# Kernel tuning notes

Measured on AMD Instinct MI355X. Metric: run time of the kernel, lower is better.

Reference implementation:

```python
import jax, jax.numpy as jnp
import numpy as np

DIM = 384          # input_dim
DI = 2 * DIM       # minGRU inner dim (expansion_factor=2)
MLP = 4 * DIM      # mlp_ratio=4
N, H, W = 32, 32, 32
EPS = 1e-5


def layer_norm(x, gamma, beta):
    mu = jnp.mean(x, axis=-1, keepdims=True)
    var = jnp.var(x, axis=-1, keepdims=True)
    return (x - mu) * jax.lax.rsqrt(var + EPS) * gamma + beta


def log_g(x):
    # log of g(x) = where(x>=0, x+0.5, sigmoid(x))
    return jnp.where(x >= 0, jnp.log(jax.nn.relu(x) + 0.5), -jax.nn.softplus(-x))


def min_gru(x, w_hg, w_out):
    # x: [n, L, d]; w_hg: [d, 2*di]; w_out: [di, d]
    hg = x @ w_hg
    hidden, gate = jnp.split(hg, 2, axis=-1)
    log_coeffs = -jax.nn.softplus(gate)            # log(1 - z)
    log_values = -jax.nn.softplus(-gate) + log_g(hidden)  # log z + log g(h~)
    # Heinsen associative scan in log space
    a_star = jnp.cumsum(log_coeffs, axis=1)
    log_h = a_star + jax.lax.cumlogsumexp(log_values - a_star, axis=1)
    return jnp.exp(log_h) @ w_out


def setup_inputs():
    key = jax.random.key(0)
    ks = jax.random.split(key, 10)
    r = lambda k, s, sc=0.02: jax.random.normal(k, s, jnp.float32) * sc
    return dict(
        x=jax.random.normal(ks[0], (N, H * W, DIM), jnp.float32),
        gamma1=jnp.ones((DIM,), jnp.float32), beta1=jnp.zeros((DIM,), jnp.float32),
        dwc_w=r(ks[1], (DIM, 1, 3, 3), 0.1), dwc_b=jnp.zeros((DIM,), jnp.float32),
        gru1_w=r(ks[2], (DIM, 2 * DI)), gru1_out=r(ks[3], (DI, DIM)),
        gru2_w=r(ks[4], (DIM, 2 * DI)), gru2_out=r(ks[5], (DI, DIM)),
        gamma2=jnp.ones((DIM,), jnp.float32), beta2=jnp.zeros((DIM,), jnp.float32),
        p1_w=r(ks[6], (DIM, MLP)), p1_b=jnp.zeros((MLP,), jnp.float32),
        p2_w=r(ks[7], (MLP, DIM)), p2_b=jnp.zeros((DIM,), jnp.float32),
        h=H, w=W,
    )


def reference(x, gamma1, beta1, dwc_w, dwc_b, gru1_w, gru1_out, gru2_w, gru2_out,
              gamma2, beta2, p1_w, p1_b, p2_w, p2_b, h, w):
    n = x.shape[0]
    residual = x
    xn = layer_norm(x, gamma1, beta1)
    # depthwise 3x3 conv on the 2D grid
    xg = xn.reshape(n, h, w, DIM).transpose(0, 3, 1, 2)  # NCHW
    xg = jax.lax.conv_general_dilated(
        xg, dwc_w, window_strides=(1, 1), padding=[(1, 1), (1, 1)],
        dimension_numbers=('NCHW', 'OIHW', 'NCHW'), feature_group_count=DIM)
    xg = xg + dwc_b[None, :, None, None]
    xs = xg.reshape(n, DIM, h * w).transpose(0, 2, 1)    # [n, hw, d]
    # bidirectional minGRU: reversed copy (flip both h and w == full seq reversal)
    x_rev = xs[:, ::-1, :]
    x1 = min_gru(xs, gru1_w, gru1_out)
    x2 = min_gru(x_rev, gru2_w, gru2_out)[:, ::-1, :]
    y = x1 + x2 + residual
    # MLP block
    residual = y
    yn = layer_norm(y, gamma2, beta2)
    yh = jax.nn.gelu(yn @ p1_w + p1_b, approximate=False)
    y = yh @ p2_w + p2_b + residual
    return y
```

## Files before the change

kernel.cpp:

```cpp
#include <hip/hip_runtime.h>
#include <hip/hip_bf16.h>

#define DIM 384
#define DI 768
#define S_LEN 1024
#define NB 32
#define M_ROWS (NB * S_LEN)
#define MLP_DIM 1536
#define CHUNKS 32
#define CLEN (S_LEN / CHUNKS)

typedef __bf16 bf16x8 __attribute__((ext_vector_type(8)));
typedef float f32x4 __attribute__((ext_vector_type(4)));

#define GLOBAL_AS __attribute__((address_space(1)))
#define LDS_AS __attribute__((address_space(3)))

template <typename OutT>
__global__ __launch_bounds__(256) void ln_kernel(const float* __restrict__ x,
                                                 const float* __restrict__ gamma,
                                                 const float* __restrict__ beta,
                                                 OutT* __restrict__ out) {
    int row = blockIdx.x * 4 + (threadIdx.x >> 6);
    int lane = threadIdx.x & 63;
    const float* xr = x + (size_t)row * DIM;
    float v[6];
    float s = 0.f, sq = 0.f;
#pragma unroll
    for (int i = 0; i < 6; ++i) {
        v[i] = xr[lane + i * 64];
        s += v[i];
        sq += v[i] * v[i];
    }
#pragma unroll
    for (int off = 32; off > 0; off >>= 1) {
        s += __shfl_down(s, off);
        sq += __shfl_down(sq, off);
    }
    s = __shfl(s, 0);
    sq = __shfl(sq, 0);
    float mean = s * (1.f / DIM);
    float var = sq * (1.f / DIM) - mean * mean;
    float rstd = rsqrtf(var + 1e-5f);
    OutT* orow = out + (size_t)row * DIM;
#pragma unroll
    for (int i = 0; i < 6; ++i) {
        int c = lane + i * 64;
        float y = (v[i] - mean) * rstd * gamma[c] + beta[c];
        if constexpr (sizeof(OutT) == 2)
            orow[c] = __float2bfloat16(y);
        else
            orow[c] = y;
    }
}

__global__ __launch_bounds__(256) void dwconv_kernel(const __hip_bfloat16* __restrict__ xn,
                                                     const float* __restrict__ w,
                                                     const float* __restrict__ b,
                                                     __hip_bfloat16* __restrict__ xs) {
    const int CB = DIM / 8;
    size_t tid = (size_t)blockIdx.x * 256 + threadIdx.x;
    int cb = (int)(tid % CB);
    int s = (int)((tid / CB) % S_LEN);
    int n = (int)(tid / ((size_t)CB * S_LEN));
    int c = cb * 8;
    int h0 = s >> 5, w0 = s & 31;

    float wv[72];
    {
        const float4* wp = (const float4*)(w + (size_t)c * 9);
#pragma unroll
        for (int i = 0; i < 18; ++i) ((float4*)wv)[i] = wp[i];
    }
    float acc[8];
    {
        const float4 b0 = *(const float4*)&b[c];
        const float4 b1 = *(const float4*)&b[c + 4];
        acc[0] = b0.x; acc[1] = b0.y; acc[2] = b0.z; acc[3] = b0.w;
        acc[4] = b1.x; acc[5] = b1.y; acc[6] = b1.z; acc[7] = b1.w;
    }

    const __hip_bfloat16* base = xn + (size_t)n * S_LEN * DIM + c;
#pragma unroll
    for (int kh = 0; kh < 3; ++kh) {
        int hh = h0 + kh - 1;
        if (hh < 0 || hh > 31) continue;
#pragma unroll
        for (int kw = 0; kw < 3; ++kw) {
            int ww = w0 + kw - 1;
            if (ww < 0 || ww > 31) continue;
            bf16x8 xv = *(const bf16x8*)&base[(size_t)(hh * 32 + ww) * DIM];
#pragma unroll
            for (int e = 0; e < 8; ++e)
                acc[e] += (float)xv[e] * wv[e * 9 + kh * 3 + kw];
        }
    }
    bf16x8 ov;
#pragma unroll
    for (int e = 0; e < 8; ++e) ov[e] = (__bf16)acc[e];
    *(bf16x8*)&xs[tid * 8] = ov;
}

__global__ __launch_bounds__(256) void transpose_bf16_kernel(const float* __restrict__ in,
                                                             __hip_bfloat16* __restrict__ out,
                                                             int R, int C, int ostride, int ooff) {
    int idx = blockIdx.x * 256 + threadIdx.x;
    if (idx >= R * C) return;
    int r = idx / C, c = idx % C;
    out[(size_t)c * ostride + ooff + r] = __float2bfloat16(in[idx]);
}

__device__ __forceinline__ void gru_ab(float hid, float gate, float& a, float& bv) {
    float z = 1.f / (1.f + __expf(-gate));
    float gh = (hid >= 0.f) ? (hid + 0.5f) : (1.f / (1.f + __expf(-hid)));
    a = 1.f - z;
    bv = z * gh;
}

__global__ __launch_bounds__(256) void scan_part1(const __hip_bfloat16* __restrict__ hg,
                                                  float* __restrict__ summ, int rev) {
    int tid = blockIdx.x * 256 + threadIdx.x;
    int c = tid % DI;
    int j = (tid / DI) % CHUNKS;
    int b = tid / (DI * CHUNKS);
    const __hip_bfloat16* base = hg + (size_t)b * S_LEN * (2 * DI);
    float A = 1.f, Bv = 0.f;
    for (int i = 0; i < CLEN; i += 8) {
        float hid[8], gate[8];
#pragma unroll
        for (int q = 0; q < 8; ++q) {
            int pos = j * CLEN + i + q;
            int t = rev ? (S_LEN - 1 - pos) : pos;
            hid[q] = __bfloat162float(base[(size_t)t * (2 * DI) + c]);
            gate[q] = __bfloat162float(base[(size_t)t * (2 * DI) + DI + c]);
        }
#pragma unroll
        for (int q = 0; q < 8; ++q) {
            float a, bv;
            gru_ab(hid[q], gate[q], a, bv);
            A *= a;
            Bv = a * Bv + bv;
        }
    }
    int idx = (j * NB + b) * DI + c;
    summ[idx] = A;
    summ[(size_t)CHUNKS * NB * DI + idx] = Bv;
}

__global__ __launch_bounds__(256) void scan_part2(const __hip_bfloat16* __restrict__ hg,
                                                  const float* __restrict__ summ,
                                                  __hip_bfloat16* __restrict__ ho, int rev,
                                                  int ostride) {
    int tid = blockIdx.x * 256 + threadIdx.x;
    int c = tid % DI;
    int j = (tid / DI) % CHUNKS;
    int b = tid / (DI * CHUNKS);
    const float* sB = summ + (size_t)CHUNKS * NB * DI;
    float h = 0.f;
    for (int jp = 0; jp < j; ++jp) {
        int idx = (jp * NB + b) * DI + c;
        h = summ[idx] * h + sB[idx];
    }
    const __hip_bfloat16* base = hg + (size_t)b * S_LEN * (2 * DI);
    __hip_bfloat16* hob = ho + (size_t)b * S_LEN * ostride;
    for (int i = 0; i < CLEN; i += 8) {
        float hid[8], gate[8];
        int tt[8];
#pragma unroll
        for (int q = 0; q < 8; ++q) {
            int pos = j * CLEN + i + q;
            int t = rev ? (S_LEN - 1 - pos) : pos;
            tt[q] = t;
            hid[q] = __bfloat162float(base[(size_t)t * (2 * DI) + c]);
            gate[q] = __bfloat162float(base[(size_t)t * (2 * DI) + DI + c]);
        }
#pragma unroll
        for (int q = 0; q < 8; ++q) {
            float a, bv;
            gru_ab(hid[q], gate[q], a, bv);
            h = a * h + bv;
            hob[(size_t)tt[q] * ostride + c] = __float2bfloat16(h);
        }
    }
}

__global__ __launch_bounds__(256) void gemm_bt(const __hip_bfloat16* __restrict__ A1, int lda1,
                                               const __hip_bfloat16* __restrict__ A2, int lda2,
                                               int ksplit,
                                               const __hip_bfloat16* __restrict__ Bt,
                                               int M, int N, int K,
                                               __hip_bfloat16* __restrict__ outH,
                                               float* __restrict__ outF,
                                               const float* __restrict__ bias,
                                               const float* __restrict__ add,
                                               int act) {
    __shared__ __align__(16) __hip_bfloat16 sA[3][128 * 32];
    __shared__ __align__(16) __hip_bfloat16 sB[3][128 * 32];
    int t = threadIdx.x;

    int nwg = gridDim.x * gridDim.y;
    int bid = blockIdx.y * gridDim.x + blockIdx.x;
    int cpx = nwg >> 3;
    int tile = (bid & 7) * cpx + (bid >> 3);
    int bx = tile % gridDim.x;
    int by = tile / gridDim.x;
    int n0 = bx * 128;
    int m0 = by * 128;

    int wave = t >> 6, lane = t & 63;
    int wm = (wave >> 1) << 6, wn = (wave & 1) << 6;
    int quad = lane >> 4, lr = lane & 15;

    f32x4 acc[4][4];
#pragma unroll
    for (int i = 0; i < 4; ++i)
#pragma unroll
        for (int j = 0; j < 4; ++j)
#pragma unroll
            for (int e = 0; e < 4; ++e) acc[i][j][e] = 0.f;

    int ch0 = wave * 128 + lane;
    int ch1 = wave * 128 + 64 + lane;
    int r0 = ch0 >> 2, g0 = (((ch0 & 3) ^ ((r0 >> 1) & 3)) * 8);
    int r1 = ch1 >> 2, g1 = (((ch1 & 3) ^ ((r1 >> 1) & 3)) * 8);
    int qx = (quad ^ ((lr >> 1) & 3)) * 8;

    const int KT = K >> 5;

    auto stage = [&](int kt) {
        int k0 = kt << 5;
        const __hip_bfloat16* Ab;
        int ldx, kk;
        if (k0 < ksplit) { Ab = A1; ldx = lda1; kk = k0; }
        else             { Ab = A2; ldx = lda2; kk = k0 - ksplit; }
        int bi = kt % 3;
        __builtin_amdgcn_global_load_lds((const GLOBAL_AS void*)(Ab + (size_t)(m0 + r0) * ldx + kk + g0),
                                         (LDS_AS void*)&sA[bi][ch0 * 8], 16, 0, 0);
        __builtin_amdgcn_global_load_lds((const GLOBAL_AS void*)(Ab + (size_t)(m0 + r1) * ldx + kk + g1),
                                         (LDS_AS void*)&sA[bi][ch1 * 8], 16, 0, 0);
        __builtin_amdgcn_global_load_lds((const GLOBAL_AS void*)(Bt + (size_t)(n0 + r0) * K + k0 + g0),
                                         (LDS_AS void*)&sB[bi][ch0 * 8], 16, 0, 0);
        __builtin_amdgcn_global_load_lds((const GLOBAL_AS void*)(Bt + (size_t)(n0 + r1) * K + k0 + g1),
                                         (LDS_AS void*)&sB[bi][ch1 * 8], 16, 0, 0);
    };

    stage(0);
    stage(1);
    for (int kt = 0; kt < KT; ++kt) {
        if (kt + 1 < KT) {
            asm volatile("s_waitcnt vmcnt(4)" ::: "memory");
        } else {
            asm volatile("s_waitcnt vmcnt(0)" ::: "memory");
        }
        __builtin_amdgcn_s_barrier();
        asm volatile("" ::: "memory");
        int bi = kt % 3;
        bf16x8 af[4], bfr[4];
#pragma unroll
        for (int mi = 0; mi < 4; ++mi)
            af[mi] = *(const bf16x8*)&sA[bi][(wm + mi * 16 + lr) * 32 + qx];
#pragma unroll
        for (int ni = 0; ni < 4; ++ni)
            bfr[ni] = *(const bf16x8*)&sB[bi][(wn + ni * 16 + lr) * 32 + qx];
        if (kt + 2 < KT) stage(kt + 2);
#pragma unroll
        for (int mi = 0; mi < 4; ++mi)
#pragma unroll
            for (int ni = 0; ni < 4; ++ni)
                acc[mi][ni] = __builtin_amdgcn_mfma_f32_16x16x32_bf16(bfr[ni], af[mi], acc[mi][ni], 0, 0, 0);
    }

#pragma unroll
    for (int mi = 0; mi < 4; ++mi) {
        int row = m0 + wm + mi * 16 + lr;
#pragma unroll
        for (int ni = 0; ni < 4; ++ni) {
            int col = n0 + wn + ni * 16 + quad * 4;
            size_t idx = (size_t)row * N + col;
            f32x4 v = acc[mi][ni];
            if (bias) {
                const float4 b4 = *(const float4*)&bias[col];
                v[0] += b4.x; v[1] += b4.y; v[2] += b4.z; v[3] += b4.w;
            }
            if (act == 1) {
#pragma unroll
                for (int e = 0; e < 4; ++e) {
                    float xv = v[e];
                    float u = 0.7978845608f * (xv + 0.044715f * xv * xv * xv);
                    float ex = __expf(2.f * u);
                    float th = (ex - 1.f) / (ex + 1.f);
                    v[e] = 0.5f * xv * (1.f + th);
                }
            }
            if (add) {
                const float4 a4 = *(const float4*)&add[idx];
                v[0] += a4.x; v[1] += a4.y; v[2] += a4.z; v[3] += a4.w;
            }
            if (outH) {
                union { __hip_bfloat16 h[4]; int2 i2; } u;
                u.h[0] = __float2bfloat16(v[0]);
                u.h[1] = __float2bfloat16(v[1]);
                u.h[2] = __float2bfloat16(v[2]);
                u.h[3] = __float2bfloat16(v[3]);
                *(int2*)&outH[idx] = u.i2;
            } else {
                *(float4*)&outF[idx] = make_float4(v[0], v[1], v[2], v[3]);
            }
        }
    }
}

extern "C" void kernel_launch(void* const* d_in, const int* in_sizes, int n_in,
                              void* d_out, int out_size, void* d_ws, size_t ws_size,
                              hipStream_t stream) {
    const float* x = (const float*)d_in[0];
    const float* gamma1 = (const float*)d_in[1];
    const float* beta1 = (const float*)d_in[2];
    const float* dwc_w = (const float*)d_in[3];
    const float* dwc_b = (const float*)d_in[4];
    const float* gru1_w = (const float*)d_in[5];
    const float* gru1_o = (const float*)d_in[6];
    const float* gru2_w = (const float*)d_in[7];
    const float* gru2_o = (const float*)d_in[8];
    const float* gamma2 = (const float*)d_in[9];
    const float* beta2 = (const float*)d_in[10];
    const float* p1_w = (const float*)d_in[11];
    const float* p1_b = (const float*)d_in[12];
    const float* p2_w = (const float*)d_in[13];
    const float* p2_b = (const float*)d_in[14];
    float* out = (float*)d_out;

    char* ws = (char*)d_ws;
    size_t off = 0;
    auto alloc = [&](size_t b) {
        char* p = ws + off;
        off += (b + 255) & ~(size_t)255;
        return p;
    };
    const size_t M = M_ROWS;
    __hip_bfloat16* hg = (__hip_bfloat16*)alloc(M * 2 * DI * 2);
    __hip_bfloat16* hbuf = (__hip_bfloat16*)alloc(M * DI * 2);
    __hip_bfloat16* xs = (__hip_bfloat16*)alloc(M * DIM * 2);
    float* summ = (float*)alloc((size_t)2 * CHUNKS * NB * DI * 4);
    __hip_bfloat16* w1T = (__hip_bfloat16*)alloc((size_t)DIM * 2 * DI * 2);
    __hip_bfloat16* w2T = (__hip_bfloat16*)alloc((size_t)DIM * 2 * DI * 2);
    __hip_bfloat16* ocT = (__hip_bfloat16*)alloc((size_t)DIM * 2 * DI * 2);
    __hip_bfloat16* p1T = (__hip_bfloat16*)alloc((size_t)DIM * MLP_DIM * 2);
    __hip_bfloat16* p2T = (__hip_bfloat16*)alloc((size_t)MLP_DIM * DIM * 2);
    __hip_bfloat16* xnb = hbuf;
    float* y = (float*)d_out;
    __hip_bfloat16* yn = xs;
    __hip_bfloat16* t1 = hg;

    auto tgrid = [](int n) { return dim3((n + 255) / 256); };
    transpose_bf16_kernel<<<tgrid(DIM * 2 * DI), 256, 0, stream>>>(gru1_w, w1T, DIM, 2 * DI, DIM, 0);
    transpose_bf16_kernel<<<tgrid(DIM * 2 * DI), 256, 0, stream>>>(gru2_w, w2T, DIM, 2 * DI, DIM, 0);
    transpose_bf16_kernel<<<tgrid(DI * DIM), 256, 0, stream>>>(gru1_o, ocT, DI, DIM, 2 * DI, 0);
    transpose_bf16_kernel<<<tgrid(DI * DIM), 256, 0, stream>>>(gru2_o, ocT, DI, DIM, 2 * DI, DI);
    transpose_bf16_kernel<<<tgrid(DIM * MLP_DIM), 256, 0, stream>>>(p1_w, p1T, DIM, MLP_DIM, DIM, 0);
    transpose_bf16_kernel<<<tgrid(MLP_DIM * DIM), 256, 0, stream>>>(p2_w, p2T, MLP_DIM, DIM, MLP_DIM, 0);

    ln_kernel<__hip_bfloat16><<<dim3(M / 4), 256, 0, stream>>>(x, gamma1, beta1, xnb);
    dwconv_kernel<<<dim3((int)((M * DIM / 8) / 256)), 256, 0, stream>>>(xnb, dwc_w, dwc_b, xs);

    const int scan_blocks = NB * CHUNKS * DI / 256;
    gemm_bt<<<dim3(2 * DI / 128, M / 128), 256, 0, stream>>>(xs, DIM, xs, DIM, DIM, w1T, M, 2 * DI, DIM,
                                                             hg, nullptr, nullptr, nullptr, 0);
    scan_part1<<<dim3(scan_blocks), 256, 0, stream>>>(hg, summ, 0);
    scan_part2<<<dim3(scan_blocks), 256, 0, stream>>>(hg, summ, hbuf, 0, DI);
    gemm_bt<<<dim3(2 * DI / 128, M / 128), 256, 0, stream>>>(xs, DIM, xs, DIM, DIM, w2T, M, 2 * DI, DIM,
                                                             hg, nullptr, nullptr, nullptr, 0);
    scan_part1<<<dim3(scan_blocks), 256, 0, stream>>>(hg, summ, 1);
    scan_part2<<<dim3(scan_blocks), 256, 0, stream>>>(hg, summ, hg, 1, 2 * DI);

    gemm_bt<<<dim3(DIM / 128, M / 128), 256, 0, stream>>>(hbuf, DI, hg, 2 * DI, DI, ocT, M, DIM, 2 * DI,
                                                          nullptr, y, nullptr, x, 0);

    ln_kernel<__hip_bfloat16><<<dim3(M / 4), 256, 0, stream>>>(y, gamma2, beta2, yn);
    gemm_bt<<<dim3(MLP_DIM / 128, M / 128), 256, 0, stream>>>(yn, DIM, yn, DIM, DIM, p1T, M, MLP_DIM, DIM,
                                                              t1, nullptr, p1_b, nullptr, 1);
    gemm_bt<<<dim3(DIM / 128, M / 128), 256, 0, stream>>>(t1, MLP_DIM, t1, MLP_DIM, MLP_DIM, p2T, M, DIM, MLP_DIM,
                                                          nullptr, out, p2_b, y, 0);
}
```

Before: 693.9 us.

## Vectorize scan kernels over 8 channels and template GEMM on K tiles

New measurement: 815.3 us. 17.5% more time.

```diff
diff --git a/kernel.cpp b/kernel.cpp
--- a/kernel.cpp
+++ b/kernel.cpp
@@ -119,81 +119,95 @@
 
 __global__ __launch_bounds__(256) void scan_part1(const __hip_bfloat16* __restrict__ hg,
                                                   float* __restrict__ summ, int rev) {
+    const int CBD = DI / 8;
     int tid = blockIdx.x * 256 + threadIdx.x;
-    int c = tid % DI;
-    int j = (tid / DI) % CHUNKS;
-    int b = tid / (DI * CHUNKS);
+    int cb = tid % CBD;
+    int j = (tid / CBD) % CHUNKS;
+    int b = tid / (CBD * CHUNKS);
+    int c = cb * 8;
     const __hip_bfloat16* base = hg + (size_t)b * S_LEN * (2 * DI);
-    float A = 1.f, Bv = 0.f;
-    for (int i = 0; i < CLEN; i += 8) {
-        float hid[8], gate[8];
-#pragma unroll
-        for (int q = 0; q < 8; ++q) {
-            int pos = j * CLEN + i + q;
-            int t = rev ? (S_LEN - 1 - pos) : pos;
-            hid[q] = __bfloat162float(base[(size_t)t * (2 * DI) + c]);
-            gate[q] = __bfloat162float(base[(size_t)t * (2 * DI) + DI + c]);
+    float A[8], Bv[8];
+#pragma unroll
+    for (int e = 0; e < 8; ++e) { A[e] = 1.f; Bv[e] = 0.f; }
+#pragma unroll 4
+    for (int i = 0; i < CLEN; ++i) {
+        int pos = j * CLEN + i;
+        int t = rev ? (S_LEN - 1 - pos) : pos;
+        bf16x8 hid = *(const bf16x8*)&base[(size_t)t * (2 * DI) + c];
+        bf16x8 gate = *(const bf16x8*)&base[(size_t)t * (2 * DI) + DI + c];
+#pragma unroll
+        for (int e = 0; e < 8; ++e) {
+            float a, bv;
+            gru_ab((float)hid[e], (float)gate[e], a, bv);
+            A[e] *= a;
+            Bv[e] = a * Bv[e] + bv;
         }
-#pragma unroll
-        for (int q = 0; q < 8; ++q) {
-            float a, bv;
-            gru_ab(hid[q], gate[q], a, bv);
-            A *= a;
-            Bv = a * Bv + bv;
-        }
     }
     int idx = (j * NB + b) * DI + c;
-    summ[idx] = A;
-    summ[(size_t)CHUNKS * NB * DI + idx] = Bv;
+    float* sB = summ + (size_t)CHUNKS * NB * DI;
+#pragma unroll
+    for (int e = 0; e < 8; e += 4) {
+        *(float4*)&summ[idx + e] = make_float4(A[e], A[e + 1], A[e + 2], A[e + 3]);
+        *(float4*)&sB[idx + e] = make_float4(Bv[e], Bv[e + 1], Bv[e + 2], Bv[e + 3]);
+    }
 }
 
 __global__ __launch_bounds__(256) void scan_part2(const __hip_bfloat16* __restrict__ hg,
                                                   const float* __restrict__ summ,
                                                   __hip_bfloat16* __restrict__ ho, int rev,
                                                   int ostride) {
+    const int CBD = DI / 8;
     int tid = blockIdx.x * 256 + threadIdx.x;
-    int c = tid % DI;
-    int j = (tid / DI) % CHUNKS;
-    int b = tid / (DI * CHUNKS);
+    int cb = tid % CBD;
+    int j = (tid / CBD) % CHUNKS;
+    int b = tid / (CBD * CHUNKS);
+    int c = cb * 8;
     const float* sB = summ + (size_t)CHUNKS * NB * DI;
-    float h = 0.f;
+    float h[8];
+#pragma unroll
+    for (int e = 0; e < 8; ++e) h[e] = 0.f;
     for (int jp = 0; jp < j; ++jp) {
         int idx = (jp * NB + b) * DI + c;
-        h = summ[idx] * h + sB[idx];
+        const float4 a0 = *(const float4*)&summ[idx];
+        const float4 a1 = *(const float4*)&summ[idx + 4];
+        const float4 b0 = *(const float4*)&sB[idx];
+        const float4 b1 = *(const float4*)&sB[idx + 4];
+        h[0] = a0.x * h[0] + b0.x; h[1] = a0.y * h[1] + b0.y;
+        h[2] = a0.z * h[2] + b0.z; h[3] = a0.w * h[3] + b0.w;
+        h[4] = a1.x * h[4] + b1.x; h[5] = a1.y * h[5] + b1.y;
+        h[6] = a1.z * h[6] + b1.z; h[7] = a1.w * h[7] + b1.w;
     }
     const __hip_bfloat16* base = hg + (size_t)b * S_LEN * (2 * DI);
     __hip_bfloat16* hob = ho + (size_t)b * S_LEN * ostride;
-    for (int i = 0; i < CLEN; i += 8) {
-        float hid[8], gate[8];
-        int tt[8];
-#pragma unroll
-        for (int q = 0; q < 8; ++q) {
-            int pos = j * CLEN + i + q;
-            int t = rev ? (S_LEN - 1 - pos) : pos;
-            tt[q] = t;
-            hid[q] = __bfloat162float(base[(size_t)t * (2 * DI) + c]);
-            gate[q] = __bfloat162float(base[(size_t)t * (2 * DI) + DI + c]);
+#pragma unroll 2
+    for (int i = 0; i < CLEN; ++i) {
+        int pos = j * CLEN + i;
+        int t = rev ? (S_LEN - 1 - pos) : pos;
+        bf16x8 hid = *(const bf16x8*)&base[(size_t)t * (2 * DI) + c];
+        bf16x8 gate = *(const bf16x8*)&base[(size_t)t * (2 * DI) + DI + c];
+        bf16x8 ov;
+#pragma unroll
+        for (int e = 0; e < 8; ++e) {
+            float a, bv;
+            gru_ab((float)hid[e], (float)gate[e], a, bv);
+            h[e] = a * h[e] + bv;
+            ov[e] = (__bf16)h[e];
         }
-#pragma unroll
-        for (int q = 0; q < 8; ++q) {
-            float a, bv;
-            gru_ab(hid[q], gate[q], a, bv);
-            h = a * h + bv;
-            hob[(size_t)tt[q] * ostride + c] = __float2bfloat16(h);
-        }
-    }
-}
-
+        *(bf16x8*)&hob[(size_t)t * ostride + c] = ov;
+    }
+}
+
+template <int KT, int KST>
 __global__ __launch_bounds__(256) void gemm_bt(const __hip_bfloat16* __restrict__ A1, int lda1,
                                                const __hip_bfloat16* __restrict__ A2, int lda2,
-                                               int ksplit,
                                                const __hip_bfloat16* __restrict__ Bt,
-                                               int M, int N, int K,
+                                               int M, int N,
                                                __hip_bfloat16* __restrict__ outH,
                                                float* __restrict__ outF,
                                                const float* __restrict__ bias,
                                                const float* __restrict__ add,
                                                int act) {
+    constexpr int K = KT * 32;
     __shared__ __align__(16) __hip_bfloat16 sA[3][128 * 32];
     __shared__ __align__(16) __hip_bfloat16 sB[3][128 * 32];
     int t = threadIdx.x;
@@ -225,27 +239,31 @@
     int r1 = ch1 >> 2, g1 = (((ch1 & 3) ^ ((r1 >> 1) & 3)) * 8);
     int qx = (quad ^ ((lr >> 1) & 3)) * 8;
 
-    const int KT = K >> 5;
+    const __hip_bfloat16* a1b0 = A1 + (size_t)(m0 + r0) * lda1 + g0;
+    const __hip_bfloat16* a1b1 = A1 + (size_t)(m0 + r1) * lda1 + g1;
+    const __hip_bfloat16* a2b0 = A2 + (size_t)(m0 + r0) * lda2 + g0;
+    const __hip_bfloat16* a2b1 = A2 + (size_t)(m0 + r1) * lda2 + g1;
+    const __hip_bfloat16* bb0 = Bt + (size_t)(n0 + r0) * K + g0;
+    const __hip_bfloat16* bb1 = Bt + (size_t)(n0 + r1) * K + g1;
 
     auto stage = [&](int kt) {
-        int k0 = kt << 5;
-        const __hip_bfloat16* Ab;
-        int ldx, kk;
-        if (k0 < ksplit) { Ab = A1; ldx = lda1; kk = k0; }
-        else             { Ab = A2; ldx = lda2; kk = k0 - ksplit; }
         int bi = kt % 3;
-        __builtin_amdgcn_global_load_lds((const GLOBAL_AS void*)(Ab + (size_t)(m0 + r0) * ldx + kk + g0),
+        const __hip_bfloat16 *pa0, *pa1;
+        if (kt < KST) { pa0 = a1b0 + kt * 32; pa1 = a1b1 + kt * 32; }
+        else          { pa0 = a2b0 + (kt - KST) * 32; pa1 = a2b1 + (kt - KST) * 32; }
+        __builtin_amdgcn_global_load_lds((const GLOBAL_AS void*)pa0,
                                          (LDS_AS void*)&sA[bi][ch0 * 8], 16, 0, 0);
-        __builtin_amdgcn_global_load_lds((const GLOBAL_AS void*)(Ab + (size_t)(m0 + r1) * ldx + kk + g1),
+        __builtin_amdgcn_global_load_lds((const GLOBAL_AS void*)pa1,
                                          (LDS_AS void*)&sA[bi][ch1 * 8], 16, 0, 0);
-        __builtin_amdgcn_global_load_lds((const GLOBAL_AS void*)(Bt + (size_t)(n0 + r0) * K + k0 + g0),
+        __builtin_amdgcn_global_load_lds((const GLOBAL_AS void*)(bb0 + kt * 32),
                                          (LDS_AS void*)&sB[bi][ch0 * 8], 16, 0, 0);
-        __builtin_amdgcn_global_load_lds((const GLOBAL_AS void*)(Bt + (size_t)(n0 + r1) * K + k0 + g1),
+        __builtin_amdgcn_global_load_lds((const GLOBAL_AS void*)(bb1 + kt * 32),
                                          (LDS_AS void*)&sB[bi][ch1 * 8], 16, 0, 0);
     };
 
     stage(0);
     stage(1);
+#pragma unroll
     for (int kt = 0; kt < KT; ++kt) {
         if (kt + 1 < KT) {
             asm volatile("s_waitcnt vmcnt(4)" ::: "memory");
@@ -363,22 +381,22 @@
     ln_kernel<__hip_bfloat16><<<dim3(M / 4), 256, 0, stream>>>(x, gamma1, beta1, xnb);
     dwconv_kernel<<<dim3((int)((M * DIM / 8) / 256)), 256, 0, stream>>>(xnb, dwc_w, dwc_b, xs);
 
-    const int scan_blocks = NB * CHUNKS * DI / 256;
-    gemm_bt<<<dim3(2 * DI / 128, M / 128), 256, 0, stream>>>(xs, DIM, xs, DIM, DIM, w1T, M, 2 * DI, DIM,
-                                                             hg, nullptr, nullptr, nullptr, 0);
+    const int scan_blocks = NB * CHUNKS * (DI / 8) / 256;
+    gemm_bt<12, 12><<<dim3(2 * DI / 128, M / 128), 256, 0, stream>>>(xs, DIM, xs, DIM, w1T, M, 2 * DI,
+                                                                     hg, nullptr, nullptr, nullptr, 0);
     scan_part1<<<dim3(scan_blocks), 256, 0, stream>>>(hg, summ, 0);
     scan_part2<<<dim3(scan_blocks), 256, 0, stream>>>(hg, summ, hbuf, 0, DI);
-    gemm_bt<<<dim3(2 * DI / 128, M / 128), 256, 0, stream>>>(xs, DIM, xs, DIM, DIM, w2T, M, 2 * DI, DIM,
-                                                             hg, nullptr, nullptr, nullptr, 0);
+    gemm_bt<12, 12><<<dim3(2 * DI / 128, M / 128), 256, 0, stream>>>(xs, DIM, xs, DIM, w2T, M, 2 * DI,
+                                                                     hg, nullptr, nullptr, nullptr, 0);
     scan_part1<<<dim3(scan_blocks), 256, 0, stream>>>(hg, summ, 1);
     scan_part2<<<dim3(scan_blocks), 256, 0, stream>>>(hg, summ, hg, 1, 2 * DI);
 
-    gemm_bt<<<dim3(DIM / 128, M / 128), 256, 0, stream>>>(hbuf, DI, hg, 2 * DI, DI, ocT, M, DIM, 2 * DI,
-                                                          nullptr, y, nullptr, x, 0);
+    gemm_bt<48, 24><<<dim3(DIM / 128, M / 128), 256, 0, stream>>>(hbuf, DI, hg, 2 * DI, ocT, M, DIM,
+                                                                  nullptr, y, nullptr, x, 0);
 
     ln_kernel<__hip_bfloat16><<<dim3(M / 4), 256, 0, stream>>>(y, gamma2, beta2, yn);
-    gemm_bt<<<dim3(MLP_DIM / 128, M / 128), 256, 0, stream>>>(yn, DIM, yn, DIM, DIM, p1T, M, MLP_DIM, DIM,
-                                                              t1, nullptr, p1_b, nullptr, 1);
-    gemm_bt<<<dim3(DIM / 128, M / 128), 256, 0, stream>>>(t1, MLP_DIM, t1, MLP_DIM, MLP_DIM, p2T, M, DIM, MLP_DIM,
-                                                          nullptr, out, p2_b, y, 0);
-}
+    gemm_bt<12, 12><<<dim3(MLP_DIM / 128, M / 128), 256, 0, stream>>>(yn, DIM, yn, DIM, p1T, M, MLP_DIM,
+                                                                      t1, nullptr, p1_b, nullptr, 1);
+    gemm_bt<48, 48><<<dim3(DIM / 128, M / 128), 256, 0, stream>>>(t1, MLP_DIM, t1, MLP_DIM, p2T, M, DIM,
+                                                                  nullptr, out, p2_b, y, 0);
+}
```

## Make short-K GEMMs persistent over M tiles and pack scan channels in pairs

Applied to the files above, without the earlier changes.

Result: slower. 733.3 us (+5.7%).

```diff
diff --git a/kernel.cpp b/kernel.cpp
--- a/kernel.cpp
+++ b/kernel.cpp
@@ -119,67 +119,83 @@
 
 __global__ __launch_bounds__(256) void scan_part1(const __hip_bfloat16* __restrict__ hg,
                                                   float* __restrict__ summ, int rev) {
+    const int CP = DI / 2;
     int tid = blockIdx.x * 256 + threadIdx.x;
-    int c = tid % DI;
-    int j = (tid / DI) % CHUNKS;
-    int b = tid / (DI * CHUNKS);
+    int cp = tid % CP;
+    int j = (tid / CP) % CHUNKS;
+    int b = tid / (CP * CHUNKS);
+    int c = cp * 2;
     const __hip_bfloat16* base = hg + (size_t)b * S_LEN * (2 * DI);
-    float A = 1.f, Bv = 0.f;
+    float A0 = 1.f, B0 = 0.f, A1 = 1.f, B1 = 0.f;
     for (int i = 0; i < CLEN; i += 8) {
-        float hid[8], gate[8];
+        unsigned hidw[8], gatew[8];
 #pragma unroll
         for (int q = 0; q < 8; ++q) {
             int pos = j * CLEN + i + q;
             int t = rev ? (S_LEN - 1 - pos) : pos;
-            hid[q] = __bfloat162float(base[(size_t)t * (2 * DI) + c]);
-            gate[q] = __bfloat162float(base[(size_t)t * (2 * DI) + DI + c]);
+            hidw[q] = *(const unsigned*)&base[(size_t)t * (2 * DI) + c];
+            gatew[q] = *(const unsigned*)&base[(size_t)t * (2 * DI) + DI + c];
         }
 #pragma unroll
         for (int q = 0; q < 8; ++q) {
             float a, bv;
-            gru_ab(hid[q], gate[q], a, bv);
-            A *= a;
-            Bv = a * Bv + bv;
-        }
-    }
-    int idx = (j * NB + b) * DI + c;
-    summ[idx] = A;
-    summ[(size_t)CHUNKS * NB * DI + idx] = Bv;
+            gru_ab(__uint_as_float(hidw[q] << 16), __uint_as_float(gatew[q] << 16), a, bv);
+            A0 *= a; B0 = a * B0 + bv;
+            gru_ab(__uint_as_float(hidw[q] & 0xffff0000u),
+                   __uint_as_float(gatew[q] & 0xffff0000u), a, bv);
+            A1 *= a; B1 = a * B1 + bv;
+        }
+    }
+    size_t idx = (size_t)(j * NB + b) * DI + c;
+    float* sB = summ + (size_t)CHUNKS * NB * DI;
+    *(float2*)&summ[idx] = make_float2(A0, A1);
+    *(float2*)&sB[idx] = make_float2(B0, B1);
 }
 
 __global__ __launch_bounds__(256) void scan_part2(const __hip_bfloat16* __restrict__ hg,
                                                   const float* __restrict__ summ,
                                                   __hip_bfloat16* __restrict__ ho, int rev,
                                                   int ostride) {
+    const int CP = DI / 2;
     int tid = blockIdx.x * 256 + threadIdx.x;
-    int c = tid % DI;
-    int j = (tid / DI) % CHUNKS;
-    int b = tid / (DI * CHUNKS);
+    int cp = tid % CP;
+    int j = (tid / CP) % CHUNKS;
+    int b = tid / (CP * CHUNKS);
+    int c = cp * 2;
     const float* sB = summ + (size_t)CHUNKS * NB * DI;
-    float h = 0.f;
+    float h0 = 0.f, h1 = 0.f;
     for (int jp = 0; jp < j; ++jp) {
-        int idx = (jp * NB + b) * DI + c;
-        h = summ[idx] * h + sB[idx];
+        size_t idx = (size_t)(jp * NB + b) * DI + c;
+        float2 a2 = *(const float2*)&summ[idx];
+        float2 b2 = *(const float2*)&sB[idx];
+        h0 = a2.x * h0 + b2.x;
+        h1 = a2.y * h1 + b2.y;
     }
     const __hip_bfloat16* base = hg + (size_t)b * S_LEN * (2 * DI);
     __hip_bfloat16* hob = ho + (size_t)b * S_LEN * ostride;
     for (int i = 0; i < CLEN; i += 8) {
-        float hid[8], gate[8];
+        unsigned hidw[8], gatew[8];
         int tt[8];
 #pragma unroll
         for (int q = 0; q < 8; ++q) {
             int pos = j * CLEN + i + q;
             int t = rev ? (S_LEN - 1 - pos) : pos;
             tt[q] = t;
-            hid[q] = __bfloat162float(base[(size_t)t * (2 * DI) + c]);
-            gate[q] = __bfloat162float(base[(size_t)t * (2 * DI) + DI + c]);
+            hidw[q] = *(const unsigned*)&base[(size_t)t * (2 * DI) + c];
+            gatew[q] = *(const unsigned*)&base[(size_t)t * (2 * DI) + DI + c];
         }
 #pragma unroll
         for (int q = 0; q < 8; ++q) {
             float a, bv;
-            gru_ab(hid[q], gate[q], a, bv);
-            h = a * h + bv;
-            hob[(size_t)tt[q] * ostride + c] = __float2bfloat16(h);
+            gru_ab(__uint_as_float(hidw[q] << 16), __uint_as_float(gatew[q] << 16), a, bv);
+            h0 = a * h0 + bv;
+            gru_ab(__uint_as_float(hidw[q] & 0xffff0000u),
+                   __uint_as_float(gatew[q] & 0xffff0000u), a, bv);
+            h1 = a * h1 + bv;
+            union { __hip_bfloat16 hh[2]; unsigned u; } o;
+            o.hh[0] = __float2bfloat16(h0);
+            o.hh[1] = __float2bfloat16(h1);
+            *(unsigned*)&hob[(size_t)tt[q] * ostride + c] = o.u;
         }
     }
 }
@@ -188,7 +204,7 @@
                                                const __hip_bfloat16* __restrict__ A2, int lda2,
                                                int ksplit,
                                                const __hip_bfloat16* __restrict__ Bt,
-                                               int M, int N, int K,
+                                               int M, int N, int K, int mtiles,
                                                __hip_bfloat16* __restrict__ outH,
                                                float* __restrict__ outF,
                                                const float* __restrict__ bias,
@@ -199,13 +215,12 @@
     int t = threadIdx.x;
 
     int nwg = gridDim.x * gridDim.y;
-    int bid = blockIdx.y * gridDim.x + blockIdx.x;
+    int pid = blockIdx.y * gridDim.x + blockIdx.x;
     int cpx = nwg >> 3;
-    int tile = (bid & 7) * cpx + (bid >> 3);
+    int tile = (pid & 7) * cpx + (pid >> 3);
     int bx = tile % gridDim.x;
-    int by = tile / gridDim.x;
+    int pby = tile / gridDim.x;
     int n0 = bx * 128;
-    int m0 = by * 128;
 
     int wave = t >> 6, lane = t & 63;
     int wm = (wave >> 1) << 6, wn = (wave & 1) << 6;
@@ -226,17 +241,23 @@
     int qx = (quad ^ ((lr >> 1) & 3)) * 8;
 
     const int KT = K >> 5;
-
-    auto stage = [&](int kt) {
-        int k0 = kt << 5;
+    const int total = KT * mtiles;
+
+    float4 bias4[4];
+    if (bias) {
+#pragma unroll
+        for (int ni = 0; ni < 4; ++ni)
+            bias4[ni] = *(const float4*)&bias[n0 + wn + ni * 16 + quad * 4];
+    }
+
+    auto stage = [&](int m0s, int k0, int bi) {
         const __hip_bfloat16* Ab;
         int ldx, kk;
         if (k0 < ksplit) { Ab = A1; ldx = lda1; kk = k0; }
         else             { Ab = A2; ldx = lda2; kk = k0 - ksplit; }
-        int bi = kt % 3;
-        __builtin_amdgcn_global_load_lds((const GLOBAL_AS void*)(Ab + (size_t)(m0 + r0) * ldx + kk + g0),
+        __builtin_amdgcn_global_load_lds((const GLOBAL_AS void*)(Ab + (size_t)(m0s + r0) * ldx + kk + g0),
                                          (LDS_AS void*)&sA[bi][ch0 * 8], 16, 0, 0);
-        __builtin_amdgcn_global_load_lds((const GLOBAL_AS void*)(Ab + (size_t)(m0 + r1) * ldx + kk + g1),
+        __builtin_amdgcn_global_load_lds((const GLOBAL_AS void*)(Ab + (size_t)(m0s + r1) * ldx + kk + g1),
                                          (LDS_AS void*)&sA[bi][ch1 * 8], 16, 0, 0);
         __builtin_amdgcn_global_load_lds((const GLOBAL_AS void*)(Bt + (size_t)(n0 + r0) * K + k0 + g0),
                                          (LDS_AS void*)&sB[bi][ch0 * 8], 16, 0, 0);
@@ -244,68 +265,95 @@
                                          (LDS_AS void*)&sB[bi][ch1 * 8], 16, 0, 0);
     };
 
-    stage(0);
-    stage(1);
-    for (int kt = 0; kt < KT; ++kt) {
-        if (kt + 1 < KT) {
-            asm volatile("s_waitcnt vmcnt(4)" ::: "memory");
-        } else {
-            asm volatile("s_waitcnt vmcnt(0)" ::: "memory");
-        }
-        __builtin_amdgcn_s_barrier();
-        asm volatile("" ::: "memory");
-        int bi = kt % 3;
-        bf16x8 af[4], bfr[4];
-#pragma unroll
-        for (int mi = 0; mi < 4; ++mi)
-            af[mi] = *(const bf16x8*)&sA[bi][(wm + mi * 16 + lr) * 32 + qx];
-#pragma unroll
-        for (int ni = 0; ni < 4; ++ni)
-            bfr[ni] = *(const bf16x8*)&sB[bi][(wn + ni * 16 + lr) * 32 + qx];
-        if (kt + 2 < KT) stage(kt + 2);
-#pragma unroll
-        for (int mi = 0; mi < 4; ++mi)
+    int s_kt = 0, s_mt = 0, s_bi = 0;
+    auto sadv = [&]() {
+        if (++s_kt == KT) { s_kt = 0; ++s_mt; }
+        if (++s_bi == 3) s_bi = 0;
+    };
+
+    stage((pby + s_mt * gridDim.y) * 128, s_kt << 5, s_bi);
+    sadv();
+    stage((pby + s_mt * gridDim.y) * 128, s_kt << 5, s_bi);
+    sadv();
+
+    int bi = 0;
+    for (int g = 0; g < mtiles; ++g) {
+        int m0 = (pby + g * gridDim.y) * 128;
+        for (int kt = 0; kt < KT; ++kt) {
+            int gk = g * KT + kt;
+            if (gk + 1 >= total) {
+                asm volatile("s_waitcnt vmcnt(0)" ::: "memory");
+            } else if (g > 0 && kt < 2) {
+                asm volatile("s_waitcnt vmcnt(20)" ::: "memory");
+            } else {
+                asm volatile("s_waitcnt vmcnt(4)" ::: "memory");
+            }
+            __builtin_amdgcn_s_barrier();
+            asm volatile("" ::: "memory");
+            bf16x8 af[4], bfr[4];
+#pragma unroll
+            for (int mi = 0; mi < 4; ++mi)
+                af[mi] = *(const bf16x8*)&sA[bi][(wm + mi * 16 + lr) * 32 + qx];
 #pragma unroll
             for (int ni = 0; ni < 4; ++ni)
-                acc[mi][ni] = __builtin_amdgcn_mfma_f32_16x16x32_bf16(bfr[ni], af[mi], acc[mi][ni], 0, 0, 0);
-    }
-
-#pragma unroll
-    for (int mi = 0; mi < 4; ++mi) {
-        int row = m0 + wm + mi * 16 + lr;
-#pragma unroll
-        for (int ni = 0; ni < 4; ++ni) {
-            int col = n0 + wn + ni * 16 + quad * 4;
-            size_t idx = (size_t)row * N + col;
-            f32x4 v = acc[mi][ni];
-            if (bias) {
-                const float4 b4 = *(const float4*)&bias[col];
-                v[0] += b4.x; v[1] += b4.y; v[2] += b4.z; v[3] += b4.w;
+                bfr[ni] = *(const bf16x8*)&sB[bi][(wn + ni * 16 + lr) * 32 + qx];
+            if (gk + 2 < total) {
+                stage((pby + s_mt * gridDim.y) * 128, s_kt << 5, s_bi);
+                sadv();
             }
-            if (act == 1) {
-#pragma unroll
-                for (int e = 0; e < 4; ++e) {
-                    float xv = v[e];
-                    float u = 0.7978845608f * (xv + 0.044715f * xv * xv * xv);
-                    float ex = __expf(2.f * u);
-                    float th = (ex - 1.f) / (ex + 1.f);
-                    v[e] = 0.5f * xv * (1.f + th);
+#pragma unroll
+            for (int mi = 0; mi < 4; ++mi)
+#pragma unroll
+                for (int ni = 0; ni < 4; ++ni)
+                    acc[mi][ni] = __builtin_amdgcn_mfma_f32_16x16x32_bf16(bfr[ni], af[mi], acc[mi][ni], 0, 0, 0);
+            if (++bi == 3) bi = 0;
+        }
+
+#pragma unroll
+        for (int mi = 0; mi < 4; ++mi) {
+            int row = m0 + wm + mi * 16 + lr;
+#pragma unroll
+            for (int ni = 0; ni < 4; ++ni) {
+                int col = n0 + wn + ni * 16 + quad * 4;
+                size_t idx = (size_t)row * N + col;
+                f32x4 v = acc[mi][ni];
+                if (bias) {
+                    v[0] += bias4[ni].x; v[1] += bias4[ni].y;
+                    v[2] += bias4[ni].z; v[3] += bias4[ni].w;
+                }
+                if (act == 1) {
+#pragma unroll
+                    for (int e = 0; e < 4; ++e) {
+                        float xv = v[e];
+                        float u = 0.7978845608f * (xv + 0.044715f * xv * xv * xv);
+                        float ex = __expf(2.f * u);
+                        float th = (ex - 1.f) / (ex + 1.f);
+                        v[e] = 0.5f * xv * (1.f + th);
+                    }
+                }
+                if (add) {
+                    const float4 a4 = *(const float4*)&add[idx];
+                    v[0] += a4.x; v[1] += a4.y; v[2] += a4.z; v[3] += a4.w;
+                }
+                if (outH) {
+                    union { __hip_bfloat16 h[4]; int2 i2; } u;
+                    u.h[0] = __float2bfloat16(v[0]);
+                    u.h[1] = __float2bfloat16(v[1]);
+                    u.h[2] = __float2bfloat16(v[2]);
+                    u.h[3] = __float2bfloat16(v[3]);
+                    *(int2*)&outH[idx] = u.i2;
+                } else {
+                    *(float4*)&outF[idx] = make_float4(v[0], v[1], v[2], v[3]);
                 }
             }
-            if (add) {
-                const float4 a4 = *(const float4*)&add[idx];
-                v[0] += a4.x; v[1] += a4.y; v[2] += a4.z; v[3] += a4.w;
-            }
-            if (outH) {
-                union { __hip_bfloat16 h[4]; int2 i2; } u;
-                u.h[0] = __float2bfloat16(v[0]);
-                u.h[1] = __float2bfloat16(v[1]);
-                u.h[2] = __float2bfloat16(v[2]);
-                u.h[3] = __float2bfloat16(v[3]);
-                *(int2*)&outH[idx] = u.i2;
-            } else {
-                *(float4*)&outF[idx] = make_float4(v[0], v[1], v[2], v[3]);
-            }
+        }
+        if (g + 1 < mtiles) {
+#pragma unroll
+            for (int i = 0; i < 4; ++i)
+#pragma unroll
+                for (int j = 0; j < 4; ++j)
+#pragma unroll
+                    for (int e = 0; e < 4; ++e) acc[i][j][e] = 0.f;
         }
     }
 }
@@ -363,22 +411,22 @@
     ln_kernel<__hip_bfloat16><<<dim3(M / 4), 256, 0, stream>>>(x, gamma1, beta1, xnb);
     dwconv_kernel<<<dim3((int)((M * DIM / 8) / 256)), 256, 0, stream>>>(xnb, dwc_w, dwc_b, xs);
 
-    const int scan_blocks = NB * CHUNKS * DI / 256;
-    gemm_bt<<<dim3(2 * DI / 128, M / 128), 256, 0, stream>>>(xs, DIM, xs, DIM, DIM, w1T, M, 2 * DI, DIM,
-                                                             hg, nullptr, nullptr, nullptr, 0);
+    const int scan_blocks = NB * CHUNKS * (DI / 2) / 256;
+    gemm_bt<<<dim3(2 * DI / 128, M / 128 / 4), 256, 0, stream>>>(xs, DIM, xs, DIM, DIM, w1T, M, 2 * DI, DIM, 4,
+                                                                 hg, nullptr, nullptr, nullptr, 0);
     scan_part1<<<dim3(scan_blocks), 256, 0, stream>>>(hg, summ, 0);
     scan_part2<<<dim3(scan_blocks), 256, 0, stream>>>(hg, summ, hbuf, 0, DI);
-    gemm_bt<<<dim3(2 * DI / 128, M / 128), 256, 0, stream>>>(xs, DIM, xs, DIM, DIM, w2T, M, 2 * DI, DIM,
-                                                             hg, nullptr, nullptr, nullptr, 0);
+    gemm_bt<<<dim3(2 * DI / 128, M / 128 / 4), 256, 0, stream>>>(xs, DIM, xs, DIM, DIM, w2T, M, 2 * DI, DIM, 4,
+                                                                 hg, nullptr, nullptr, nullptr, 0);
     scan_part1<<<dim3(scan_blocks), 256, 0, stream>>>(hg, summ, 1);
     scan_part2<<<dim3(scan_blocks), 256, 0, stream>>>(hg, summ, hg, 1, 2 * DI);
 
-    gemm_bt<<<dim3(DIM / 128, M / 128), 256, 0, stream>>>(hbuf, DI, hg, 2 * DI, DI, ocT, M, DIM, 2 * DI,
+    gemm_bt<<<dim3(DIM / 128, M / 128), 256, 0, stream>>>(hbuf, DI, hg, 2 * DI, DI, ocT, M, DIM, 2 * DI, 1,
                                                           nullptr, y, nullptr, x, 0);
 
     ln_kernel<__hip_bfloat16><<<dim3(M / 4), 256, 0, stream>>>(y, gamma2, beta2, yn);
-    gemm_bt<<<dim3(MLP_DIM / 128, M / 128), 256, 0, stream>>>(yn, DIM, yn, DIM, DIM, p1T, M, MLP_DIM, DIM,
-                                                              t1, nullptr, p1_b, nullptr, 1);
-    gemm_bt<<<dim3(DIM / 128, M / 128), 256, 0, stream>>>(t1, MLP_DIM, t1, MLP_DIM, MLP_DIM, p2T, M, DIM, MLP_DIM,
+    gemm_bt<<<dim3(MLP_DIM / 128, M / 128 / 4), 256, 0, stream>>>(yn, DIM, yn, DIM, DIM, p1T, M, MLP_DIM, DIM, 4,
+                                                                  t1, nullptr, p1_b, nullptr, 1);
+    gemm_bt<<<dim3(DIM / 128, M / 128), 256, 0, stream>>>(t1, MLP_DIM, t1, MLP_DIM, MLP_DIM, p2T, M, DIM, MLP_DIM, 1,
                                                           nullptr, out, p2_b, y, 0);
 }
```
